# Kernel optimization log

Hardware: AMD Instinct MI355X
Metric: run time of the kernel (lower is better)

Reference implementation:

```python
import jax, jax.numpy as jnp
import numpy as np
from jax import lax

EPS = 1e-5
DN = ('NCHW', 'OIHW', 'NCHW')


def setup_inputs() -> dict:
    key = jax.random.key(0)
    ks = jax.random.split(key, 16)
    B = 8192
    # uniform(0,1): every pixel nonzero => all voxels active => sparse conv == dense conv
    x = jax.random.uniform(ks[0], (B, 1, 28, 28), dtype=jnp.float32)

    def conv_params(kw, kb, c_in, c_out, k):
        scale = 1.0 / np.sqrt(c_in * k * k)
        w = jax.random.normal(kw, (c_out, c_in, k, k), dtype=jnp.float32) * scale
        b = jax.random.normal(kb, (c_out,), dtype=jnp.float32) * scale
        return w, b

    w0, b0 = conv_params(ks[1], ks[2], 1, 32, 3)
    w1, b1 = conv_params(ks[3], ks[4], 32, 64, 2)
    w2, b2 = conv_params(ks[5], ks[6], 64, 128, 2)
    # BatchNorm affine params (init: gamma=1, beta=0)
    g0, be0 = jnp.ones((32,), jnp.float32), jnp.zeros((32,), jnp.float32)
    g1, be1 = jnp.ones((64,), jnp.float32), jnp.zeros((64,), jnp.float32)
    g2, be2 = jnp.ones((128,), jnp.float32), jnp.zeros((128,), jnp.float32)
    w_fc = jax.random.normal(ks[7], (10, 128), dtype=jnp.float32) * (1.0 / np.sqrt(128))
    b_fc = jax.random.normal(ks[8], (10,), dtype=jnp.float32) * (1.0 / np.sqrt(128))
    return dict(x=x, w0=w0, b0=b0, g0=g0, be0=be0,
                w1=w1, b1=b1, g1=g1, be1=be1,
                w2=w2, b2=b2, g2=g2, be2=be2,
                w_fc=w_fc, b_fc=b_fc)


def _conv_bn_relu(x, w, b, g, be, stride, padding):
    # sparse conv on fully-active grid == dense conv
    y = lax.conv_general_dilated(x, w, (stride, stride), padding,
                                 dimension_numbers=DN)
    y = y + b[None, :, None, None]
    # BatchNorm1d over (N_active, C) == stats over batch+spatial (biased var)
    mean = jnp.mean(y, axis=(0, 2, 3))
    var = jnp.var(y, axis=(0, 2, 3))
    y = (y - mean[None, :, None, None]) * lax.rsqrt(var + EPS)[None, :, None, None]
    y = y * g[None, :, None, None] + be[None, :, None, None]
    return jax.nn.relu(y)


def reference(x, w0, b0, g0, be0, w1, b1, g1, be1, w2, b2, g2, be2, w_fc, b_fc):
    h = _conv_bn_relu(x, w0, b0, g0, be0, 1, 'SAME')    # (B,32,28,28)
    h = _conv_bn_relu(h, w1, b1, g1, be1, 2, 'VALID')   # (B,64,14,14)
    h = _conv_bn_relu(h, w2, b2, g2, be2, 2, 'VALID')   # (B,128,7,7)
    pooled = jnp.mean(h, axis=(2, 3))                    # AdaptiveAvgPool2d(1)+Flatten
    return pooled @ w_fc.T + b_fc                        # (B, n_classes)
```

## Files before the change

kernel.cpp:

```cpp
#include <hip/hip_runtime.h>
#include <hip/hip_bf16.h>

typedef __bf16 bf16x8 __attribute__((ext_vector_type(8)));
typedef float  f32x4  __attribute__((ext_vector_type(4)));

#define BSZ 8192

union BW2 { __bf16 b[2]; unsigned int u; };
union FR  { unsigned int u[4]; bf16x8 v; };

__global__ __launch_bounds__(256) void k_stats0(const float* __restrict__ x,
                                                float* __restrict__ part0,
                                                const float* __restrict__ w1,
                                                const float* __restrict__ w2,
                                                __bf16* __restrict__ w1b,
                                                __bf16* __restrict__ w2b) {
    __shared__ float sred[4 * 54];
    const int tid = threadIdx.x;
    {
        int t = blockIdx.x * 256 + tid;
        if (t < 8192) {
            int oc = t >> 7, k = t & 127, c = k & 31, d = k >> 5;
            w1b[t] = (__bf16)w1[oc * 128 + c * 4 + d];
        }
        if (t < 32768) {
            int oc = t >> 8, k = t & 255, c = k & 63, d = k >> 6;
            w2b[t] = (__bf16)w2[oc * 256 + c * 4 + d];
        }
    }
    float a[54];
#pragma unroll
    for (int i = 0; i < 54; i++) a[i] = 0.f;
    const int total = BSZ * 784;
    for (int p = blockIdx.x * 256 + tid; p < total; p += gridDim.x * 256) {
        int b = p / 784, pix = p - b * 784;
        int y = pix / 28, xx = pix - y * 28;
        const float* xb = x + (long)b * 784;
        float nv[9];
#pragma unroll
        for (int dy = 0; dy < 3; dy++) {
            int yy = y + dy - 1;
#pragma unroll
            for (int dx = 0; dx < 3; dx++) {
                int x2 = xx + dx - 1;
                nv[dy * 3 + dx] = (yy >= 0 && yy < 28 && x2 >= 0 && x2 < 28) ? xb[yy * 28 + x2] : 0.f;
            }
        }
        int idx = 0;
#pragma unroll
        for (int t2 = 0; t2 < 9; t2++) {
            float vt = nv[t2];
            a[45 + t2] += vt;
#pragma unroll
            for (int u = t2; u < 9; u++) { a[idx] += vt * nv[u]; idx++; }
        }
    }
#pragma unroll
    for (int i = 0; i < 54; i++) {
        float v = a[i];
        v += __shfl_xor(v, 1);  v += __shfl_xor(v, 2);  v += __shfl_xor(v, 4);
        v += __shfl_xor(v, 8);  v += __shfl_xor(v, 16); v += __shfl_xor(v, 32);
        a[i] = v;
    }
    const int l = tid & 63, w = tid >> 6;
    if (l == 0) {
#pragma unroll
        for (int i = 0; i < 54; i++) sred[w * 54 + i] = a[i];
    }
    __syncthreads();
    if (tid < 54)
        part0[blockIdx.x * 64 + tid] = sred[tid] + sred[54 + tid] + sred[108 + tid] + sred[162 + tid];
}

__global__ void k_fin0(const float* __restrict__ part0, const float* __restrict__ w0,
                       const float* __restrict__ g0, const float* __restrict__ be0,
                       float* __restrict__ abc0, __bf16* __restrict__ wcv) {
    __shared__ float red[4 * 54];
    int t = threadIdx.x, c = t & 63, g = t >> 6;
    if (c < 54) {
        float acc = 0.f;
        for (int i = g; i < 1008; i += 4) acc += part0[i * 64 + c];
        red[g * 54 + c] = acc;
    }
    __syncthreads();
    if (t < 54) red[t] = red[t] + red[54 + t] + red[108 + t] + red[162 + t];
    __syncthreads();
    if (t < 32) {
        float wv[9];
#pragma unroll
        for (int tap = 0; tap < 9; tap++) wv[tap] = w0[t * 9 + tap];
        float sum = 0.f, sq = 0.f;
        int idx = 0;
#pragma unroll
        for (int ta = 0; ta < 9; ta++) {
            sum = fmaf(wv[ta], red[45 + ta], sum);
#pragma unroll
            for (int u = ta; u < 9; u++) {
                float coef = (u == ta) ? 1.f : 2.f;
                sq = fmaf(coef * wv[ta] * wv[u], red[idx], sq);
                idx++;
            }
        }
        float cnt = (float)BSZ * 784.f;
        float mean = sum / cnt;
        float var = sq / cnt - mean * mean;
        float A = g0[t] * rsqrtf(var + 1e-5f);
        abc0[288 + t] = be0[t] - mean * A;
        int nn = t >> 1, hh = t & 1;
#pragma unroll
        for (int j = 0; j < 4; j++) {
#pragma unroll
            for (int e = 0; e < 8; e++) {
                float vm = 0.f, vc = 0.f;
                if (j < 3) {
                    int i = e >> 1;
                    if (i < 3) vm = A * wv[j * 3 + i];
                    if (e < 3) {
                        float wfull = A * wv[j * 3 + e];
                        vc = wfull - (float)((__bf16)wfull);
                    }
                }
                wcv[hh * 512 + j * 128 + nn * 8 + e]       = (__bf16)vm;
                wcv[(2 + hh) * 512 + j * 128 + nn * 8 + e] = (__bf16)vc;
            }
        }
    }
}

__global__ __launch_bounds__(256, 4) void k_conv01(const float* __restrict__ x,
                                                   const float* __restrict__ abc0,
                                                   const __bf16* __restrict__ wcv,
                                                   const __bf16* __restrict__ w1b,
                                                   __bf16* __restrict__ h1,
                                                   float* __restrict__ part1) {
    __shared__ unsigned int xs2[31 * 30];
    __shared__ __attribute__((aligned(16))) __bf16 sAt[2][16 * 136];
    const int tid = threadIdx.x;
    const int w = tid >> 6, l = tid & 63, q = l >> 4, n = l & 15;
    const int d1 = w >> 1, d0 = w & 1;
    for (int i = tid; i < 930; i += 256) xs2[i] = 0u;
    bf16x8 bw[2][2];
#pragma unroll
    for (int ps = 0; ps < 2; ps++)
#pragma unroll
        for (int h = 0; h < 2; h++)
            bw[ps][h] = *(const bf16x8*)&wcv[(ps * 2 + h) * 512 + q * 128 + n * 8];
    const float bias0 = abc0[288 + 2 * n];
    const float bias1 = abc0[288 + 2 * n + 1];
    const int oc = w * 16 + n;
    bf16x8 fbv[4];
#pragma unroll
    for (int kc = 0; kc < 4; kc++)
        fbv[kc] = *(const bf16x8*)&w1b[oc * 128 + kc * 32 + q * 8];
    __syncthreads();

    for (int img = 0; img < 4; img++) {
        const int b = blockIdx.x * 4 + img;
        for (int jj = tid; jj < 784; jj += 256) {
            int yy = jj / 28, xx2 = jj - yy * 28;
            float f = x[(long)b * 784 + jj];
            __bf16 hi = (__bf16)f;
            __bf16 lo = (__bf16)(f - (float)hi);
            BW2 pk; pk.b[0] = hi; pk.b[1] = lo;
            xs2[(yy + 1) * 30 + xx2 + 1] = pk.u;
        }
        __syncthreads();
        float ssum = 0.f, ssq = 0.f;
        __bf16* hb = h1 + (long)b * 12544 + (q * 4) * 64 + oc;
        for (int mt = 0; mt < 13; mt++) {
            {
                int m = mt * 16 + n;
                int mv = m < 195 ? m : 195;
                int my = mv / 14, mx = mv - my * 14;
                int row = 2 * my + d1 + q, col = 2 * mx + d0;
                const unsigned int* p = &xs2[row * 30 + col];
                unsigned int u0 = p[0], u1 = p[1], u2 = p[2];
                FR a0, a1;
                a0.u[0] = u0; a0.u[1] = u1; a0.u[2] = u2; a0.u[3] = 0u;
                a1.u[0] = (u0 & 0xffffu) | (u1 << 16); a1.u[1] = u2 & 0xffffu;
                a1.u[2] = 0u; a1.u[3] = 0u;
                f32x4 ac0 = {bias0, bias0, bias0, bias0};
                f32x4 ac1 = {bias1, bias1, bias1, bias1};
                ac0 = __builtin_amdgcn_mfma_f32_16x16x32_bf16(a0.v, bw[0][0], ac0, 0, 0, 0);
                ac1 = __builtin_amdgcn_mfma_f32_16x16x32_bf16(a0.v, bw[0][1], ac1, 0, 0, 0);
                ac0 = __builtin_amdgcn_mfma_f32_16x16x32_bf16(a1.v, bw[1][0], ac0, 0, 0, 0);
                ac1 = __builtin_amdgcn_mfma_f32_16x16x32_bf16(a1.v, bw[1][1], ac1, 0, 0, 0);
#pragma unroll
                for (int r = 0; r < 4; r++) {
                    int mrow = q * 4 + r;
                    float v0 = fmaxf(ac0[r], 0.f), v1 = fmaxf(ac1[r], 0.f);
                    if (mt * 16 + mrow >= 196) { v0 = 0.f; v1 = 0.f; }
                    BW2 pk; pk.b[0] = (__bf16)v0; pk.b[1] = (__bf16)v1;
                    *(unsigned int*)&sAt[mt & 1][mrow * 136 + w * 32 + 2 * n] = pk.u;
                }
            }
            __syncthreads();
            const __bf16* sa = &sAt[mt & 1][n * 136 + q * 8];
            f32x4 acc = {0.f, 0.f, 0.f, 0.f};
#pragma unroll
            for (int kc = 0; kc < 4; kc++) {
                bf16x8 fav = *(const bf16x8*)&sa[kc * 32];
                acc = __builtin_amdgcn_mfma_f32_16x16x32_bf16(fav, fbv[kc], acc, 0, 0, 0);
            }
            bool valid = (mt < 12) | (q == 0);
            __bf16* hp = hb + mt * 16 * 64;
#pragma unroll
            for (int r = 0; r < 4; r++) {
                __bf16 hv = (__bf16)acc[r];
                if (valid) hp[r * 64] = hv;
                float fv = (float)hv;
                ssum += fv; ssq += fv * fv;
            }
        }
        ssum += __shfl_xor(ssum, 16); ssum += __shfl_xor(ssum, 32);
        ssq  += __shfl_xor(ssq, 16);  ssq  += __shfl_xor(ssq, 32);
        if (l < 16) {
            part1[(long)oc * BSZ + b] = ssum;
            part1[(long)(64 + oc) * BSZ + b] = ssq;
        }
    }
}

__global__ __launch_bounds__(256) void k_redfin(const float* __restrict__ part,
                                                const float* __restrict__ g,
                                                const float* __restrict__ be,
                                                float* __restrict__ abc,
                                                int C, float cnt) {
    __shared__ float s1[256], s2[256];
    const int c = blockIdx.x, tid = threadIdx.x;
    float a = 0.f, bq = 0.f;
    const float* p1 = part + (long)c * BSZ;
    const float* p2 = part + (long)(C + c) * BSZ;
    for (int i = tid; i < BSZ; i += 256) { a += p1[i]; bq += p2[i]; }
    s1[tid] = a; s2[tid] = bq;
    __syncthreads();
    for (int s = 128; s > 0; s >>= 1) {
        if (tid < s) { s1[tid] += s1[tid + s]; s2[tid] += s2[tid + s]; }
        __syncthreads();
    }
    if (tid == 0) {
        float mean = s1[0] / cnt;
        float var = s2[0] / cnt - mean * mean;
        float A = g[c] * rsqrtf(var + 1e-5f);
        abc[c] = A;
        abc[C + c] = be[c] - mean * A;
    }
}

__global__ __launch_bounds__(256) void k_conv2s(__bf16* __restrict__ h1,
                                                const __bf16* __restrict__ w2b,
                                                const float* __restrict__ abc1,
                                                float* __restrict__ part2) {
    __shared__ __attribute__((aligned(16))) __bf16 sAt[2][16 * 264];
    __shared__ __attribute__((aligned(16))) __bf16 zt[16 * 136];
    __shared__ float sbn1[128];
    const int tid = threadIdx.x;
    if (tid < 128) sbn1[tid] = abc1[tid];
    const int w = tid >> 6, l = tid & 63, q = l >> 4, n = l & 15;
    bf16x8 fbv[2][8];
#pragma unroll
    for (int ntl = 0; ntl < 2; ntl++) {
        int oc = (2 * w + ntl) * 16 + n;
#pragma unroll
        for (int kc = 0; kc < 8; kc++)
            fbv[ntl][kc] = *(const bf16x8*)&w2b[oc * 256 + kc * 32 + q * 8];
    }
    __syncthreads();

    for (int img = 0; img < 4; img++) {
        const int b = blockIdx.x * 4 + img;
        __bf16* src = h1 + (long)b * 12544;
        float ssum[2] = {0.f, 0.f}, ssq[2] = {0.f, 0.f};
        for (int mt = 0; mt < 4; mt++) {
#pragma unroll
            for (int it = 0; it < 2; it++) {
                int idx = it * 256 + tid;
                int rl = idx >> 5, o = (idx & 31) * 8;
                int r = mt * 16 + rl;
                bf16x8 wv;
                if (r < 49) {
                    int d = o >> 6, c = o & 63;
                    int py = r / 7, px = r - py * 7;
                    int msrc = (2 * py + (d >> 1)) * 14 + 2 * px + (d & 1);
                    bf16x8 v = *(const bf16x8*)&src[msrc * 64 + c];
#pragma unroll
                    for (int j = 0; j < 8; j++) {
                        float f = fmaxf((float)v[j] * sbn1[c + j] + sbn1[64 + c + j], 0.f);
                        wv[j] = (__bf16)f;
                    }
                } else {
#pragma unroll
                    for (int j = 0; j < 8; j++) wv[j] = (__bf16)0.0f;
                }
                *(bf16x8*)&sAt[mt & 1][rl * 264 + o] = wv;
            }
            __syncthreads();
            bf16x8 fav[8];
#pragma unroll
            for (int kc = 0; kc < 8; kc++)
                fav[kc] = *(const bf16x8*)&sAt[mt & 1][n * 264 + kc * 32 + q * 8];
#pragma unroll
            for (int ntl = 0; ntl < 2; ntl++) {
                f32x4 acc = {0.f, 0.f, 0.f, 0.f};
#pragma unroll
                for (int kc = 0; kc < 8; kc++)
                    acc = __builtin_amdgcn_mfma_f32_16x16x32_bf16(fav[kc], fbv[ntl][kc], acc, 0, 0, 0);
#pragma unroll
                for (int rr = 0; rr < 4; rr++) {
                    __bf16 hv = (__bf16)acc[rr];
                    zt[(q * 4 + rr) * 136 + (2 * w + ntl) * 16 + n] = hv;
                    float fv = (float)hv;
                    ssum[ntl] += fv; ssq[ntl] += fv * fv;
                }
            }
            __syncthreads();
            {
                int row = tid >> 4, o = (tid & 15) * 8;
                int m = mt * 16 + row;
                if (m < 49) {
                    bf16x8 zv = *(const bf16x8*)&zt[row * 136 + o];
                    *(bf16x8*)&src[m * 128 + o] = zv;
                }
            }
        }
#pragma unroll
        for (int ntl = 0; ntl < 2; ntl++) {
            ssum[ntl] += __shfl_xor(ssum[ntl], 16); ssum[ntl] += __shfl_xor(ssum[ntl], 32);
            ssq[ntl]  += __shfl_xor(ssq[ntl], 16);  ssq[ntl]  += __shfl_xor(ssq[ntl], 32);
        }
        if (l < 16) {
#pragma unroll
            for (int ntl = 0; ntl < 2; ntl++) {
                int oc = (2 * w + ntl) * 16 + l;
                part2[(long)oc * BSZ + b] = ssum[ntl];
                part2[(long)(128 + oc) * BSZ + b] = ssq[ntl];
            }
        }
    }
}

__global__ __launch_bounds__(256) void k_final(const __bf16* __restrict__ z2,
                                               const float* __restrict__ abc2,
                                               const float* __restrict__ wfc,
                                               const float* __restrict__ bfc,
                                               float* __restrict__ out) {
    __shared__ float sbn2[256];
    __shared__ float pp[16 * 128];
    __shared__ float pooled[128];
    __shared__ float fcred[80];
    const int tid = threadIdx.x;
    sbn2[tid] = abc2[tid];
    __syncthreads();
    const int g = tid & 15, c0 = g * 8, rg = tid >> 4;
    for (int img = 0; img < 4; img++) {
        const int b = blockIdx.x * 4 + img;
        const __bf16* src = z2 + (long)b * 12544;
        float acc[8];
#pragma unroll
        for (int q = 0; q < 8; q++) acc[q] = 0.f;
        for (int rr = rg; rr < 49; rr += 16) {
            bf16x8 v = *(const bf16x8*)&src[rr * 128 + c0];
#pragma unroll
            for (int q = 0; q < 8; q++) {
                float f = fmaxf((float)v[q] * sbn2[c0 + q] + sbn2[128 + c0 + q], 0.f);
                acc[q] += f;
            }
        }
        *(f32x4*)&pp[rg * 128 + c0]     = *(f32x4*)&acc[0];
        *(f32x4*)&pp[rg * 128 + c0 + 4] = *(f32x4*)&acc[4];
        __syncthreads();
        if (tid < 128) {
            float s = 0.f;
#pragma unroll
            for (int r = 0; r < 16; r++) s += pp[r * 128 + tid];
            pooled[tid] = s * (1.f / 49.f);
        }
        __syncthreads();
        if (tid < 80) {
            int o = tid >> 3, s = tid & 7;
            float a = 0.f;
#pragma unroll
            for (int j = 0; j < 16; j++) a = fmaf(pooled[s * 16 + j], wfc[o * 128 + s * 16 + j], a);
            fcred[tid] = a;
        }
        __syncthreads();
        if (tid < 10) {
            float a = bfc[tid];
#pragma unroll
            for (int s = 0; s < 8; s++) a += fcred[tid * 8 + s];
            out[(long)b * 10 + tid] = a;
        }
    }
}

extern "C" void kernel_launch(void* const* d_in, const int* in_sizes, int n_in,
                              void* d_out, int out_size, void* d_ws, size_t ws_size,
                              hipStream_t stream) {
    const float* x   = (const float*)d_in[0];
    const float* w0  = (const float*)d_in[1];
    const float* g0  = (const float*)d_in[3];
    const float* be0 = (const float*)d_in[4];
    const float* w1  = (const float*)d_in[5];
    const float* g1  = (const float*)d_in[7];
    const float* be1 = (const float*)d_in[8];
    const float* w2  = (const float*)d_in[9];
    const float* g2  = (const float*)d_in[11];
    const float* be2 = (const float*)d_in[12];
    const float* wfc = (const float*)d_in[13];
    const float* bfc = (const float*)d_in[14];
    float* out = (float*)d_out;

    float* ws    = (float*)d_ws;
    float* part0 = ws;
    __bf16* wcv  = (__bf16*)(part0 + 1008 * 64);
    float* abc0  = part0 + 1024 * 64;
    float* part1 = abc0 + 320;
    float* abc1  = part1 + 128 * BSZ;
    float* part2 = abc1 + 128;
    float* abc2  = part2 + 256 * BSZ;
    __bf16* w1b  = (__bf16*)(abc2 + 256);
    __bf16* w2b  = w1b + 8192;
    __bf16* h1   = w2b + 32768;

    k_stats0<<<dim3(1008), dim3(256), 0, stream>>>(x, part0, w1, w2, w1b, w2b);
    k_fin0<<<dim3(1), dim3(256), 0, stream>>>(part0, w0, g0, be0, abc0, wcv);
    k_conv01<<<dim3(BSZ / 4), dim3(256), 0, stream>>>(x, abc0, wcv, w1b, h1, part1);
    k_redfin<<<dim3(64), dim3(256), 0, stream>>>(part1, g1, be1, abc1, 64, (float)(BSZ * 196));
    k_conv2s<<<dim3(BSZ / 4), dim3(256), 0, stream>>>(h1, w2b, abc1, part2);
    k_redfin<<<dim3(128), dim3(256), 0, stream>>>(part2, g2, be2, abc2, 128, (float)(BSZ * 49));
    k_final<<<dim3(BSZ / 4), dim3(256), 0, stream>>>(h1, abc2, wfc, bfc, out);
}
```

Baseline: 389.3 us.

## Run conv01 as one wave per image and interleave conv2 MFMA chains

k_conv01 now launches one 64-thread wave per image instead of four waves sharing four images. Each wave computes all four stride phases and all 64 output channels itself. This removes the per-tile __syncthreads and the double-buffered LDS tile, and adds s_setprio around the MFMA section. BN statistics are now accumulated from the fp32 accumulators rather than the bf16-rounded values. In k_conv2s the channel-to-lane mapping changes so that two independent MFMA accumulator chains interleave and the results go to LDS as packed bf16 pairs. This trades higher register pressure and a single-wave workgroup for the loss of block-level sync overhead.

Measured after the change: 388.3 us. About the same (-0.3%).

```diff
diff --git a/kernel.cpp b/kernel.cpp
--- a/kernel.cpp
+++ b/kernel.cpp
@@ -127,18 +127,18 @@
     }
 }
 
-__global__ __launch_bounds__(256, 4) void k_conv01(const float* __restrict__ x,
-                                                   const float* __restrict__ abc0,
-                                                   const __bf16* __restrict__ wcv,
-                                                   const __bf16* __restrict__ w1b,
-                                                   __bf16* __restrict__ h1,
-                                                   float* __restrict__ part1) {
+__global__ __launch_bounds__(64, 3) void k_conv01(const float* __restrict__ x,
+                                                  const float* __restrict__ abc0,
+                                                  const __bf16* __restrict__ wcv,
+                                                  const __bf16* __restrict__ w1b,
+                                                  __bf16* __restrict__ h1,
+                                                  float* __restrict__ part1) {
     __shared__ unsigned int xs2[31 * 30];
-    __shared__ __attribute__((aligned(16))) __bf16 sAt[2][16 * 136];
-    const int tid = threadIdx.x;
-    const int w = tid >> 6, l = tid & 63, q = l >> 4, n = l & 15;
-    const int d1 = w >> 1, d0 = w & 1;
-    for (int i = tid; i < 930; i += 256) xs2[i] = 0u;
+    __shared__ __attribute__((aligned(16))) __bf16 sAt[16 * 136];
+    const int l = threadIdx.x;
+    const int q = l >> 4, n = l & 15;
+    const int b = blockIdx.x;
+    for (int i = l; i < 930; i += 64) xs2[i] = 0u;
     bf16x8 bw[2][2];
 #pragma unroll
     for (int ps = 0; ps < 2; ps++)
@@ -147,76 +147,96 @@
             bw[ps][h] = *(const bf16x8*)&wcv[(ps * 2 + h) * 512 + q * 128 + n * 8];
     const float bias0 = abc0[288 + 2 * n];
     const float bias1 = abc0[288 + 2 * n + 1];
-    const int oc = w * 16 + n;
-    bf16x8 fbv[4];
-#pragma unroll
-    for (int kc = 0; kc < 4; kc++)
-        fbv[kc] = *(const bf16x8*)&w1b[oc * 128 + kc * 32 + q * 8];
-    __syncthreads();
-
-    for (int img = 0; img < 4; img++) {
-        const int b = blockIdx.x * 4 + img;
-        for (int jj = tid; jj < 784; jj += 256) {
-            int yy = jj / 28, xx2 = jj - yy * 28;
-            float f = x[(long)b * 784 + jj];
-            __bf16 hi = (__bf16)f;
-            __bf16 lo = (__bf16)(f - (float)hi);
-            BW2 pk; pk.b[0] = hi; pk.b[1] = lo;
-            xs2[(yy + 1) * 30 + xx2 + 1] = pk.u;
-        }
-        __syncthreads();
-        float ssum = 0.f, ssq = 0.f;
-        __bf16* hb = h1 + (long)b * 12544 + (q * 4) * 64 + oc;
-        for (int mt = 0; mt < 13; mt++) {
-            {
-                int m = mt * 16 + n;
-                int mv = m < 195 ? m : 195;
-                int my = mv / 14, mx = mv - my * 14;
-                int row = 2 * my + d1 + q, col = 2 * mx + d0;
-                const unsigned int* p = &xs2[row * 30 + col];
-                unsigned int u0 = p[0], u1 = p[1], u2 = p[2];
-                FR a0, a1;
-                a0.u[0] = u0; a0.u[1] = u1; a0.u[2] = u2; a0.u[3] = 0u;
-                a1.u[0] = (u0 & 0xffffu) | (u1 << 16); a1.u[1] = u2 & 0xffffu;
-                a1.u[2] = 0u; a1.u[3] = 0u;
-                f32x4 ac0 = {bias0, bias0, bias0, bias0};
-                f32x4 ac1 = {bias1, bias1, bias1, bias1};
-                ac0 = __builtin_amdgcn_mfma_f32_16x16x32_bf16(a0.v, bw[0][0], ac0, 0, 0, 0);
-                ac1 = __builtin_amdgcn_mfma_f32_16x16x32_bf16(a0.v, bw[0][1], ac1, 0, 0, 0);
-                ac0 = __builtin_amdgcn_mfma_f32_16x16x32_bf16(a1.v, bw[1][0], ac0, 0, 0, 0);
-                ac1 = __builtin_amdgcn_mfma_f32_16x16x32_bf16(a1.v, bw[1][1], ac1, 0, 0, 0);
-#pragma unroll
-                for (int r = 0; r < 4; r++) {
-                    int mrow = q * 4 + r;
-                    float v0 = fmaxf(ac0[r], 0.f), v1 = fmaxf(ac1[r], 0.f);
-                    if (mt * 16 + mrow >= 196) { v0 = 0.f; v1 = 0.f; }
-                    BW2 pk; pk.b[0] = (__bf16)v0; pk.b[1] = (__bf16)v1;
-                    *(unsigned int*)&sAt[mt & 1][mrow * 136 + w * 32 + 2 * n] = pk.u;
-                }
-            }
-            __syncthreads();
-            const __bf16* sa = &sAt[mt & 1][n * 136 + q * 8];
+    bf16x8 fbv[4][4];
+#pragma unroll
+    for (int g = 0; g < 4; g++)
+#pragma unroll
+        for (int kc = 0; kc < 4; kc++)
+            fbv[g][kc] = *(const bf16x8*)&w1b[(g * 16 + n) * 128 + kc * 32 + q * 8];
+
+    for (int jj = l; jj < 784; jj += 64) {
+        int yy = jj / 28, xx2 = jj - yy * 28;
+        float f = x[(long)b * 784 + jj];
+        __bf16 hi = (__bf16)f;
+        __bf16 lo = (__bf16)(f - (float)hi);
+        BW2 pk; pk.b[0] = hi; pk.b[1] = lo;
+        xs2[(yy + 1) * 30 + xx2 + 1] = pk.u;
+    }
+
+    float ssum[4], ssq[4];
+#pragma unroll
+    for (int g = 0; g < 4; g++) { ssum[g] = 0.f; ssq[g] = 0.f; }
+    int my = (n >= 14) ? 1 : 0;
+    int mx = n - my * 14;
+    __bf16* hb = h1 + (long)b * 12544 + q * 256 + n;
+
+    auto produce = [&](int mt, bool last) {
+        int myv = my, mxv = mx;
+        if (last) {
+            bool pad = (n >= 4);
+            myv = pad ? 13 : my;
+            mxv = pad ? 13 : mx;
+        }
+        const int rowb = 2 * myv + q, colb = 2 * mxv;
+#pragma unroll
+        for (int t = 0; t < 4; t++) {
+            const int d1 = t >> 1, d0 = t & 1;
+            const unsigned int* p = &xs2[(rowb + d1) * 30 + colb + d0];
+            unsigned int u0 = p[0], u1 = p[1], u2 = p[2];
+            FR a0, a1;
+            a0.u[0] = u0; a0.u[1] = u1; a0.u[2] = u2; a0.u[3] = 0u;
+            a1.u[0] = (u0 & 0xffffu) | (u1 << 16); a1.u[1] = u2 & 0xffffu;
+            a1.u[2] = 0u; a1.u[3] = 0u;
+            f32x4 ac0 = {bias0, bias0, bias0, bias0};
+            f32x4 ac1 = {bias1, bias1, bias1, bias1};
+            ac0 = __builtin_amdgcn_mfma_f32_16x16x32_bf16(a0.v, bw[0][0], ac0, 0, 0, 0);
+            ac1 = __builtin_amdgcn_mfma_f32_16x16x32_bf16(a0.v, bw[0][1], ac1, 0, 0, 0);
+            ac0 = __builtin_amdgcn_mfma_f32_16x16x32_bf16(a1.v, bw[1][0], ac0, 0, 0, 0);
+            ac1 = __builtin_amdgcn_mfma_f32_16x16x32_bf16(a1.v, bw[1][1], ac1, 0, 0, 0);
+#pragma unroll
+            for (int r = 0; r < 4; r++) {
+                float v0 = fmaxf(ac0[r], 0.f), v1 = fmaxf(ac1[r], 0.f);
+                if (last && q != 0) { v0 = 0.f; v1 = 0.f; }
+                BW2 pk; pk.b[0] = (__bf16)v0; pk.b[1] = (__bf16)v1;
+                *(unsigned int*)&sAt[(q * 4 + r) * 136 + t * 32 + 2 * n] = pk.u;
+            }
+        }
+    };
+
+    for (int mt = 0; mt < 13; mt++) {
+        if (mt < 12) produce(mt, false); else produce(mt, true);
+        mx += 2; my += 1;
+        if (mx >= 14) { mx -= 14; my += 1; }
+        bf16x8 fav[4];
+        const __bf16* sa = &sAt[n * 136 + q * 8];
+#pragma unroll
+        for (int kc = 0; kc < 4; kc++) fav[kc] = *(const bf16x8*)&sa[kc * 32];
+        const bool valid = (mt < 12) | (q == 0);
+        __builtin_amdgcn_s_setprio(1);
+#pragma unroll
+        for (int g = 0; g < 4; g++) {
             f32x4 acc = {0.f, 0.f, 0.f, 0.f};
 #pragma unroll
-            for (int kc = 0; kc < 4; kc++) {
-                bf16x8 fav = *(const bf16x8*)&sa[kc * 32];
-                acc = __builtin_amdgcn_mfma_f32_16x16x32_bf16(fav, fbv[kc], acc, 0, 0, 0);
-            }
-            bool valid = (mt < 12) | (q == 0);
-            __bf16* hp = hb + mt * 16 * 64;
+            for (int kc = 0; kc < 4; kc++)
+                acc = __builtin_amdgcn_mfma_f32_16x16x32_bf16(fav[kc], fbv[g][kc], acc, 0, 0, 0);
 #pragma unroll
             for (int r = 0; r < 4; r++) {
-                __bf16 hv = (__bf16)acc[r];
-                if (valid) hp[r * 64] = hv;
-                float fv = (float)hv;
-                ssum += fv; ssq += fv * fv;
-            }
-        }
-        ssum += __shfl_xor(ssum, 16); ssum += __shfl_xor(ssum, 32);
-        ssq  += __shfl_xor(ssq, 16);  ssq  += __shfl_xor(ssq, 32);
-        if (l < 16) {
-            part1[(long)oc * BSZ + b] = ssum;
-            part1[(long)(64 + oc) * BSZ + b] = ssq;
+                if (valid) hb[mt * 1024 + r * 64 + g * 16] = (__bf16)acc[r];
+                ssum[g] += acc[r]; ssq[g] += acc[r] * acc[r];
+            }
+        }
+        __builtin_amdgcn_s_setprio(0);
+    }
+#pragma unroll
+    for (int g = 0; g < 4; g++) {
+        ssum[g] += __shfl_xor(ssum[g], 16); ssum[g] += __shfl_xor(ssum[g], 32);
+        ssq[g]  += __shfl_xor(ssq[g], 16);  ssq[g]  += __shfl_xor(ssq[g], 32);
+    }
+    if (l < 16) {
+#pragma unroll
+        for (int g = 0; g < 4; g++) {
+            part1[(long)(g * 16 + l) * BSZ + b] = ssum[g];
+            part1[(long)(64 + g * 16 + l) * BSZ + b] = ssq[g];
         }
     }
 }
@@ -260,7 +280,7 @@
     bf16x8 fbv[2][8];
 #pragma unroll
     for (int ntl = 0; ntl < 2; ntl++) {
-        int oc = (2 * w + ntl) * 16 + n;
+        int oc = w * 32 + 2 * n + ntl;
 #pragma unroll
         for (int kc = 0; kc < 8; kc++)
             fbv[ntl][kc] = *(const bf16x8*)&w2b[oc * 256 + kc * 32 + q * 8];
@@ -299,19 +319,18 @@
 #pragma unroll
             for (int kc = 0; kc < 8; kc++)
                 fav[kc] = *(const bf16x8*)&sAt[mt & 1][n * 264 + kc * 32 + q * 8];
-#pragma unroll
-            for (int ntl = 0; ntl < 2; ntl++) {
-                f32x4 acc = {0.f, 0.f, 0.f, 0.f};
-#pragma unroll
-                for (int kc = 0; kc < 8; kc++)
-                    acc = __builtin_amdgcn_mfma_f32_16x16x32_bf16(fav[kc], fbv[ntl][kc], acc, 0, 0, 0);
-#pragma unroll
-                for (int rr = 0; rr < 4; rr++) {
-                    __bf16 hv = (__bf16)acc[rr];
-                    zt[(q * 4 + rr) * 136 + (2 * w + ntl) * 16 + n] = hv;
-                    float fv = (float)hv;
-                    ssum[ntl] += fv; ssq[ntl] += fv * fv;
-                }
+            f32x4 accA = {0.f, 0.f, 0.f, 0.f}, accB = {0.f, 0.f, 0.f, 0.f};
+#pragma unroll
+            for (int kc = 0; kc < 8; kc++) {
+                accA = __builtin_amdgcn_mfma_f32_16x16x32_bf16(fav[kc], fbv[0][kc], accA, 0, 0, 0);
+                accB = __builtin_amdgcn_mfma_f32_16x16x32_bf16(fav[kc], fbv[1][kc], accB, 0, 0, 0);
+            }
+#pragma unroll
+            for (int rr = 0; rr < 4; rr++) {
+                BW2 pk; pk.b[0] = (__bf16)accA[rr]; pk.b[1] = (__bf16)accB[rr];
+                *(unsigned int*)&zt[(q * 4 + rr) * 136 + w * 32 + 2 * n] = pk.u;
+                ssum[0] += accA[rr]; ssq[0] += accA[rr] * accA[rr];
+                ssum[1] += accB[rr]; ssq[1] += accB[rr] * accB[rr];
             }
             __syncthreads();
             {
@@ -331,7 +350,7 @@
         if (l < 16) {
 #pragma unroll
             for (int ntl = 0; ntl < 2; ntl++) {
-                int oc = (2 * w + ntl) * 16 + l;
+                int oc = w * 32 + 2 * l + ntl;
                 part2[(long)oc * BSZ + b] = ssum[ntl];
                 part2[(long)(128 + oc) * BSZ + b] = ssq[ntl];
             }
@@ -424,7 +443,7 @@
 
     k_stats0<<<dim3(1008), dim3(256), 0, stream>>>(x, part0, w1, w2, w1b, w2b);
     k_fin0<<<dim3(1), dim3(256), 0, stream>>>(part0, w0, g0, be0, abc0, wcv);
-    k_conv01<<<dim3(BSZ / 4), dim3(256), 0, stream>>>(x, abc0, wcv, w1b, h1, part1);
+    k_conv01<<<dim3(BSZ), dim3(64), 0, stream>>>(x, abc0, wcv, w1b, h1, part1);
     k_redfin<<<dim3(64), dim3(256), 0, stream>>>(part1, g1, be1, abc1, 64, (float)(BSZ * 196));
     k_conv2s<<<dim3(BSZ / 4), dim3(256), 0, stream>>>(h1, w2b, abc1, part2);
     k_redfin<<<dim3(128), dim3(256), 0, stream>>>(part2, g2, be2, abc2, 128, (float)(BSZ * 49));
```
